# Optimization experiments

Measured on AMD Instinct MI355X. Metric: run time of the kernel, lower is better.

## Reference

```python
import jax, jax.numpy as jnp
import numpy as np
from jax import lax

BATCH, SEQ, IN_DIM, STATE, OUT_DIM = 8, 4096, 256, 256, 256


def setup_inputs() -> dict:
    key = jax.random.key(0)
    kx, ka, kb, kc = jax.random.split(key, 4)
    x = jax.random.normal(kx, (BATCH, SEQ, IN_DIM), dtype=jnp.float32)
    # A initialized as randn normalized by its largest singular value (spectral norm)
    A_init = jax.random.normal(ka, (STATE, STATE), dtype=jnp.float32)
    s_max = jnp.linalg.svd(A_init, compute_uv=False)[0]
    A = A_init / (s_max + 1e-8)
    B = jax.random.normal(kb, (IN_DIM, STATE), dtype=jnp.float32) / IN_DIM
    C = jax.random.normal(kc, (STATE, OUT_DIM), dtype=jnp.float32) / STATE
    h0 = jnp.zeros((STATE,), dtype=jnp.float32)
    return {"x": x, "A": A, "B": B, "C": C, "h0": h0}


def reference(x, A, B, C, h0):
    # h_{t} = h_{t-1} @ A + x_t @ B ;  y_t = h_t @ C
    bsz = x.shape[0]
    xB = jnp.einsum('bsi,in->sbn', x, B)  # precompute input projections, time-major
    h_init = jnp.broadcast_to(h0, (bsz, h0.shape[0]))

    def step(h, xb_t):
        h = h @ A + xb_t
        return h, h

    _, hs = lax.scan(step, h_init, xB)  # hs: [S, B, N]
    y = jnp.einsum('sbn,no->bso', hs, C)  # [B, S, O]
    return y
```

## Files before the change

### kernel.cpp

```cpp
#include <hip/hip_runtime.h>


#define SEQ    4096
#define NBATCH 8
#define ND     256
#define CHUNK  8
#define NCHUNK 512
#define GSZ    16
#define NGRP   32
#define LOSC   2048.0f
#define LOINV  (1.0f/2048.0f)

typedef _Float16 fp16_t;
typedef __attribute__((ext_vector_type(8))) _Float16 f16x8;
typedef __attribute__((ext_vector_type(4))) _Float16 f16x4;
typedef __attribute__((ext_vector_type(4))) float f32x4;

__global__ __launch_bounds__(64) void prep_frags3(
    const float* __restrict__ A, const float* __restrict__ B,
    const float* __restrict__ C,
    fp16_t* __restrict__ fAh, fp16_t* __restrict__ fAl,
    fp16_t* __restrict__ fBh, fp16_t* __restrict__ fBl,
    fp16_t* __restrict__ fCh, fp16_t* __restrict__ fCl) {
  const int which = blockIdx.x >> 7;
  const int blk   = blockIdx.x & 127;
  const float* M = (which == 0) ? A : (which == 1) ? B : C;
  fp16_t* hi = (which == 0) ? fAh : (which == 1) ? fBh : fCh;
  fp16_t* lo = (which == 0) ? fAl : (which == 1) ? fBl : fCl;
  const int lane = threadIdx.x;
  const int tile = blk >> 3, slice = blk & 7;
  const int n  = tile * 16 + (lane & 15);
  const int k0 = slice * 32 + (lane >> 4) * 8;
  f16x8 vh, vl;
  #pragma unroll
  for (int j = 0; j < 8; ++j) {
    const float v = M[(size_t)(k0 + j) * ND + n];
    const fp16_t h = (fp16_t)v;
    vh[j] = h;
    vl[j] = (fp16_t)((v - (float)h) * LOSC);
  }
  const size_t fo = ((size_t)blk * 64 + lane) * 8;
  *(f16x8*)&hi[fo] = vh;
  *(f16x8*)&lo[fo] = vl;
}

__global__ __launch_bounds__(64) void prep_frags2(
    const float* __restrict__ M0, const float* __restrict__ M1,
    fp16_t* __restrict__ h0p, fp16_t* __restrict__ l0p,
    fp16_t* __restrict__ h1p, fp16_t* __restrict__ l1p) {
  const int which = blockIdx.x >> 7;
  const int blk   = blockIdx.x & 127;
  const float* M = (which == 0) ? M0 : M1;
  fp16_t* hi = (which == 0) ? h0p : h1p;
  fp16_t* lo = (which == 0) ? l0p : l1p;
  const int lane = threadIdx.x;
  const int tile = blk >> 3, slice = blk & 7;
  const int n  = tile * 16 + (lane & 15);
  const int k0 = slice * 32 + (lane >> 4) * 8;
  f16x8 vh, vl;
  #pragma unroll
  for (int j = 0; j < 8; ++j) {
    const float v = M[(size_t)(k0 + j) * ND + n];
    const fp16_t h = (fp16_t)v;
    vh[j] = h;
    vl[j] = (fp16_t)((v - (float)h) * LOSC);
  }
  const size_t fo = ((size_t)blk * 64 + lane) * 8;
  *(f16x8*)&hi[fo] = vh;
  *(f16x8*)&lo[fo] = vl;
}

__global__ __launch_bounds__(1024, 4) void mfma_gemm(const float* __restrict__ X,
                                                     const fp16_t* __restrict__ Mhi,
                                                     const fp16_t* __restrict__ Mlo,
                                                     float* __restrict__ Out,
                                                     int mode) {
  const int m0   = blockIdx.x * 64;
  const int tid  = threadIdx.x;
  const int lane = tid & 63;
  const int w    = tid >> 6;
  const int br   = lane & 15;
  const int akg  = lane >> 4;

  __shared__ fp16_t Xh[64 * ND];
  __shared__ fp16_t Xl[64 * ND];
  char* Xhb = (char*)Xh;
  char* Xlb = (char*)Xl;

  {
    const int r0   = tid >> 6;
    const int col0 = (tid & 63) * 4;
    #pragma unroll
    for (int rr = 0; rr < 4; ++rr) {
      const int row = rr * 16 + r0;
      const int m = m0 + row;
      const size_t in_row = (mode == 0)
          ? ((size_t)(m & 7) * SEQ + (m >> 3))
          : (size_t)m;
      const float4 xv = *(const float4*)&X[in_row * ND + col0];
      const float a[4] = {xv.x, xv.y, xv.z, xv.w};
      f16x4 vh, vl;
      #pragma unroll
      for (int j = 0; j < 4; ++j) {
        const fp16_t h = (fp16_t)a[j];
        vh[j] = h;
        vl[j] = (fp16_t)((a[j] - (float)h) * LOSC);
      }
      const int byte = (row * 512 + col0 * 2) ^ ((row & 7) << 4);
      *(f16x4*)(Xhb + byte) = vh;
      *(f16x4*)(Xlb + byte) = vl;
    }
  }

  f16x8 MH[8], ML[8];
  #pragma unroll
  for (int s = 0; s < 8; ++s) {
    const size_t fo = (((size_t)w * 8 + s) * 64 + lane) * 8;
    MH[s] = *(const f16x8*)&Mhi[fo];
    ML[s] = *(const f16x8*)&Mlo[fo];
  }
  __syncthreads();

  f32x4 accm[4], accl[4];
  #pragma unroll
  for (int mt = 0; mt < 4; ++mt) {
    accm[mt] = (f32x4)0.0f;
    accl[mt] = (f32x4)0.0f;
  }

  #pragma unroll
  for (int s = 0; s < 8; ++s) {
    #pragma unroll
    for (int mt = 0; mt < 4; ++mt) {
      const int row = mt * 16 + br;
      const int byte = (row * 512 + s * 64 + akg * 16) ^ ((row & 7) << 4);
      const f16x8 bh = *(const f16x8*)(Xhb + byte);
      const f16x8 bl = *(const f16x8*)(Xlb + byte);
      accm[mt] = __builtin_amdgcn_mfma_f32_16x16x32_f16(MH[s], bh, accm[mt], 0, 0, 0);
      accl[mt] = __builtin_amdgcn_mfma_f32_16x16x32_f16(ML[s], bh, accl[mt], 0, 0, 0);
      accl[mt] = __builtin_amdgcn_mfma_f32_16x16x32_f16(MH[s], bl, accl[mt], 0, 0, 0);
    }
  }

  #pragma unroll
  for (int mt = 0; mt < 4; ++mt) {
    const int m = m0 + mt * 16 + br;
    const size_t out_row = (mode == 1)
        ? ((size_t)(m & 7) * SEQ + (m >> 3))
        : (size_t)m;
    float4 o;
    o.x = accm[mt][0] + accl[mt][0] * LOINV;
    o.y = accm[mt][1] + accl[mt][1] * LOINV;
    o.z = accm[mt][2] + accl[mt][2] * LOINV;
    o.w = accm[mt][3] + accl[mt][3] * LOINV;
    *(float4*)&Out[out_row * ND + w * 16 + akg * 4] = o;
  }
}

__global__ __launch_bounds__(1024, 4) void mfma_rscan(
    const fp16_t* __restrict__ Mh, const fp16_t* __restrict__ Ml,
    const float* __restrict__ Init,
    const float* In,
    float* OutEach,
    float* __restrict__ OutFinal,
    int nupd, int gstride, int nseq, int init_bcast, int entry_mode) {
  const int seq0 = blockIdx.x * 2;
  const int tid  = threadIdx.x;
  const int lane = tid & 63;
  const int w    = tid >> 6;
  const int br   = lane & 15;
  const int akg  = lane >> 4;

  __shared__ fp16_t hH[16 * ND];
  __shared__ fp16_t hL[16 * ND];
  char* hHb = (char*)hH;
  char* hLb = (char*)hL;

  {
    const int row  = tid >> 6;
    const int col0 = (tid & 63) * 4;
    const int sq = seq0 + (row >> 3);
    const int b  = row & 7;
    float4 v = make_float4(0.f, 0.f, 0.f, 0.f);
    if (Init != nullptr && sq < nseq) {
      const size_t off = init_bcast ? (size_t)col0
                                    : ((size_t)sq * NBATCH + b) * ND + col0;
      v = *(const float4*)&Init[off];
      if (entry_mode && OutEach != nullptr)
        *(float4*)&OutEach[((size_t)sq * gstride * NBATCH + b) * ND + col0] = v;
    }
    const float a[4] = {v.x, v.y, v.z, v.w};
    f16x4 vh, vl;
    #pragma unroll
    for (int j = 0; j < 4; ++j) {
      const fp16_t h = (fp16_t)a[j];
      vh[j] = h;
      vl[j] = (fp16_t)((a[j] - (float)h) * LOSC);
    }
    const int byte = (row * 512 + col0 * 2) ^ ((row & 7) << 4);
    *(f16x4*)(hHb + byte) = vh;
    *(f16x4*)(hLb + byte) = vl;
  }

  f16x8 AH[8], AL[8];
  #pragma unroll
  for (int s = 0; s < 8; ++s) {
    const size_t fo = (((size_t)w * 8 + s) * 64 + lane) * 8;
    AH[s] = *(const f16x8*)&Mh[fo];
    AL[s] = *(const f16x8*)&Ml[fo];
  }
  __syncthreads();

  const int sq   = seq0 + (br >> 3);
  const int b    = br & 7;
  const bool live = (sq < nseq);
  const int sqc  = live ? sq : (nseq - 1);
  const int col0 = w * 16 + akg * 4;

  float4 uv = *(const float4*)&In[((size_t)(sqc * gstride) * NBATCH + b) * ND + col0];
  float4 uvn;
  f32x4 res;
  for (int j = 0; j < nupd; ++j) {
    if (j + 1 < nupd)
      uvn = *(const float4*)&In[((size_t)(sqc * gstride + j + 1) * NBATCH + b) * ND + col0];
    f32x4 accm, accl;
    accm[0] = uv.x; accm[1] = uv.y; accm[2] = uv.z; accm[3] = uv.w;
    accl = (f32x4)0.0f;
    #pragma unroll
    for (int s = 0; s < 8; ++s) {
      const int byte = (br * 512 + s * 64 + akg * 16) ^ ((br & 7) << 4);
      const f16x8 bh = *(const f16x8*)(hHb + byte);
      const f16x8 bl = *(const f16x8*)(hLb + byte);
      accm = __builtin_amdgcn_mfma_f32_16x16x32_f16(AH[s], bh, accm, 0, 0, 0);
      accl = __builtin_amdgcn_mfma_f32_16x16x32_f16(AL[s], bh, accl, 0, 0, 0);
      accl = __builtin_amdgcn_mfma_f32_16x16x32_f16(AH[s], bl, accl, 0, 0, 0);
    }
    #pragma unroll
    for (int r = 0; r < 4; ++r) res[r] = accm[r] + accl[r] * LOINV;
    __syncthreads();
    {
      f16x4 vh, vl;
      #pragma unroll
      for (int r = 0; r < 4; ++r) {
        const fp16_t hh = (fp16_t)res[r];
        vh[r] = hh;
        vl[r] = (fp16_t)((res[r] - (float)hh) * LOSC);
      }
      const int wb = (br * 512 + col0 * 2) ^ ((br & 7) << 4);
      *(f16x4*)(hHb + wb) = vh;
      *(f16x4*)(hLb + wb) = vl;
    }
    if (OutEach != nullptr && live) {
      const size_t pos = entry_mode ? (size_t)(sq * gstride + j + 1)
                                    : (size_t)(sq * gstride + j);
      float4 o;
      o.x = res[0]; o.y = res[1]; o.z = res[2]; o.w = res[3];
      *(float4*)&OutEach[(pos * NBATCH + b) * ND + col0] = o;
    }
    uv = uvn;
    __syncthreads();
  }

  if (OutFinal != nullptr && live) {
    float4 o;
    o.x = res[0]; o.y = res[1]; o.z = res[2]; o.w = res[3];
    *(float4*)&OutFinal[((size_t)sq * NBATCH + b) * ND + col0] = o;
  }
}

__global__ __launch_bounds__(256) void gemm256(const float* __restrict__ X,
                                               const float* __restrict__ Y,
                                               float* __restrict__ Out) {
  const int m0 = blockIdx.x * 4;
  const int n  = threadIdx.x;
  __shared__ float Xs[ND][4];
  #pragma unroll
  for (int r = 0; r < 4; ++r) Xs[n][r] = X[(m0 + r) * ND + n];
  __syncthreads();
  float a0 = 0.f, a1 = 0.f, a2 = 0.f, a3 = 0.f;
  #pragma unroll 8
  for (int k = 0; k < ND; ++k) {
    const float yv = Y[k * ND + n];
    const float4 xv = *(const float4*)&Xs[k][0];
    a0 = fmaf(xv.x, yv, a0);
    a1 = fmaf(xv.y, yv, a1);
    a2 = fmaf(xv.z, yv, a2);
    a3 = fmaf(xv.w, yv, a3);
  }
  Out[(m0 + 0) * ND + n] = a0;
  Out[(m0 + 1) * ND + n] = a1;
  Out[(m0 + 2) * ND + n] = a2;
  Out[(m0 + 3) * ND + n] = a3;
}

extern "C" void kernel_launch(void* const* d_in, const int* in_sizes, int n_in,
                              void* d_out, int out_size, void* d_ws, size_t ws_size,
                              hipStream_t stream) {
  const float* x  = (const float*)d_in[0];
  const float* A  = (const float*)d_in[1];
  const float* Bm = (const float*)d_in[2];
  const float* Cm = (const float*)d_in[3];
  const float* h0 = (const float*)d_in[4];
  float* y = (float*)d_out;

  float* U    = (float*)d_ws;
  float* t0   = U + (size_t)SEQ * NBATCH * ND;
  float* t1   = t0 + ND * ND;
  float* A8   = t1 + ND * ND;
  float* A128 = A8 + ND * ND;
  float* E    = A128 + ND * ND;
  float* Sg   = E + (size_t)NCHUNK * NBATCH * ND;
  float* G    = Sg + (size_t)NGRP * NBATCH * ND;
  float* Hc   = G + (size_t)NGRP * NBATCH * ND;
  fp16_t* fA_hi = (fp16_t*)(Hc + (size_t)NCHUNK * NBATCH * ND);
  fp16_t* fA_lo = fA_hi + ND * ND;
  fp16_t* fB_hi = fA_lo + ND * ND;
  fp16_t* fB_lo = fB_hi + ND * ND;
  fp16_t* fC_hi = fB_lo + ND * ND;
  fp16_t* fC_lo = fC_hi + ND * ND;
  fp16_t* fA8_hi   = (fp16_t*)t0;
  fp16_t* fA8_lo   = fA8_hi + ND * ND;
  fp16_t* fA128_hi = (fp16_t*)t1;
  fp16_t* fA128_lo = fA128_hi + ND * ND;

  prep_frags3<<<384, 64, 0, stream>>>(A, Bm, Cm, fA_hi, fA_lo, fB_hi, fB_lo,
                                      fC_hi, fC_lo);

  gemm256<<<64, 256, 0, stream>>>(A,  A,  t0);
  gemm256<<<64, 256, 0, stream>>>(t0, t0, t1);
  gemm256<<<64, 256, 0, stream>>>(t1, t1, A8);
  gemm256<<<64, 256, 0, stream>>>(A8, A8, t0);
  gemm256<<<64, 256, 0, stream>>>(t0, t0, t1);
  gemm256<<<64, 256, 0, stream>>>(t1, t1, t0);
  gemm256<<<64, 256, 0, stream>>>(t0, t0, A128);

  prep_frags2<<<256, 64, 0, stream>>>(A8, A128, fA8_hi, fA8_lo,
                                      fA128_hi, fA128_lo);

  mfma_gemm<<<512, 1024, 0, stream>>>(x, fB_hi, fB_lo, U, 0);

  mfma_rscan<<<NCHUNK / 2, 1024, 0, stream>>>(fA_hi, fA_lo, nullptr, U,
                                              nullptr, E, CHUNK, CHUNK,
                                              NCHUNK, 0, 0);

  mfma_rscan<<<NGRP / 2, 1024, 0, stream>>>(fA8_hi, fA8_lo, nullptr, E,
                                            nullptr, Sg, GSZ, GSZ, NGRP, 0, 0);

  mfma_rscan<<<1, 1024, 0, stream>>>(fA128_hi, fA128_lo, h0, Sg,
                                     G, nullptr, NGRP - 1, NGRP, 1, 1, 1);

  mfma_rscan<<<NGRP / 2, 1024, 0, stream>>>(fA8_hi, fA8_lo, G, E,
                                            Hc, nullptr, GSZ - 1, GSZ, NGRP,
                                            0, 1);

  mfma_rscan<<<NCHUNK / 2, 1024, 0, stream>>>(fA_hi, fA_lo, Hc, U,
                                              U, nullptr, CHUNK, CHUNK,
                                              NCHUNK, 0, 0);

  mfma_gemm<<<512, 1024, 0, stream>>>(U, fC_hi, fC_lo, y, 1);
}
```

Measured before the change: 258.8 us.

## Double-buffer scan state in LDS and re-layout fragments for MFMA reads

The recurrent scan kernel now ping-pongs the fp16 hi/lo state between two LDS buffers, which removes one of the two __syncthreads per step. It also splits the low-part accumulator into two independent chains to shorten the MFMA dependency chain. Both the GEMM and scan kernels change their LDS layout to a per-k-slice, XOR-swizzled fragment-major form so each lane reads a contiguous 16-byte fragment, and the GEMM staging loads 8 floats per thread. The launch-bound occupancy hint is lowered from 4 to 2, which gives the compiler more registers per thread but may reduce residency.

```diff
diff --git a/kernel.cpp b/kernel.cpp
--- a/kernel.cpp
+++ b/kernel.cpp
@@ -70,7 +70,7 @@
   *(f16x8*)&lo[fo] = vl;
 }
 
-__global__ __launch_bounds__(1024, 4) void mfma_gemm(const float* __restrict__ X,
+__global__ __launch_bounds__(1024, 2) void mfma_gemm(const float* __restrict__ X,
                                                      const fp16_t* __restrict__ Mhi,
                                                      const fp16_t* __restrict__ Mlo,
                                                      float* __restrict__ Out,
@@ -82,34 +82,37 @@
   const int br   = lane & 15;
   const int akg  = lane >> 4;
 
-  __shared__ fp16_t Xh[64 * ND];
-  __shared__ fp16_t Xl[64 * ND];
+  __shared__ fp16_t Xh[32 * 512];
+  __shared__ fp16_t Xl[32 * 512];
   char* Xhb = (char*)Xh;
   char* Xlb = (char*)Xl;
 
-  {
-    const int r0   = tid >> 6;
-    const int col0 = (tid & 63) * 4;
-    #pragma unroll
-    for (int rr = 0; rr < 4; ++rr) {
-      const int row = rr * 16 + r0;
-      const int m = m0 + row;
-      const size_t in_row = (mode == 0)
-          ? ((size_t)(m & 7) * SEQ + (m >> 3))
-          : (size_t)m;
-      const float4 xv = *(const float4*)&X[in_row * ND + col0];
-      const float a[4] = {xv.x, xv.y, xv.z, xv.w};
-      f16x4 vh, vl;
-      #pragma unroll
-      for (int j = 0; j < 4; ++j) {
-        const fp16_t h = (fp16_t)a[j];
-        vh[j] = h;
-        vl[j] = (fp16_t)((a[j] - (float)h) * LOSC);
-      }
-      const int byte = (row * 512 + col0 * 2) ^ ((row & 7) << 4);
-      *(f16x4*)(Xhb + byte) = vh;
-      *(f16x4*)(Xlb + byte) = vl;
-    }
+  #pragma unroll
+  for (int pass = 0; pass < 2; ++pass) {
+    const int tau = pass * 1024 + tid;
+    const int row = tau >> 5;
+    const int sub = tau & 31;
+    const int s   = sub >> 2;
+    const int ak  = sub & 3;
+    const int m = m0 + row;
+    const size_t in_row = (mode == 0)
+        ? ((size_t)(m & 7) * SEQ + (m >> 3))
+        : (size_t)m;
+    const float* xp = &X[in_row * ND + s * 32 + ak * 8];
+    const float4 x0 = *(const float4*)(xp);
+    const float4 x1 = *(const float4*)(xp + 4);
+    const float a[8] = {x0.x, x0.y, x0.z, x0.w, x1.x, x1.y, x1.z, x1.w};
+    f16x8 vh, vl;
+    #pragma unroll
+    for (int j = 0; j < 8; ++j) {
+      const fp16_t h = (fp16_t)a[j];
+      vh[j] = h;
+      vl[j] = (fp16_t)((a[j] - (float)h) * LOSC);
+    }
+    const int off = (((row >> 4) * 8 + s) << 10) +
+                    (((ak << 4) | (row & 15)) ^ s) * 16;
+    *(f16x8*)(Xhb + off) = vh;
+    *(f16x8*)(Xlb + off) = vl;
   }
 
   f16x8 MH[8], ML[8];
@@ -128,18 +131,20 @@
     accl[mt] = (f32x4)0.0f;
   }
 
+  const int rdslot = (((akg << 4) | br)) * 16;
   #pragma unroll
   for (int s = 0; s < 8; ++s) {
+    const int rdoff = (s ^ ((rdslot >> 4) & 0)) ;
     #pragma unroll
     for (int mt = 0; mt < 4; ++mt) {
-      const int row = mt * 16 + br;
-      const int byte = (row * 512 + s * 64 + akg * 16) ^ ((row & 7) << 4);
+      const int byte = ((mt * 8 + s) << 10) + ((((akg << 4) | br) ^ s) << 4);
       const f16x8 bh = *(const f16x8*)(Xhb + byte);
       const f16x8 bl = *(const f16x8*)(Xlb + byte);
       accm[mt] = __builtin_amdgcn_mfma_f32_16x16x32_f16(MH[s], bh, accm[mt], 0, 0, 0);
       accl[mt] = __builtin_amdgcn_mfma_f32_16x16x32_f16(ML[s], bh, accl[mt], 0, 0, 0);
       accl[mt] = __builtin_amdgcn_mfma_f32_16x16x32_f16(MH[s], bl, accl[mt], 0, 0, 0);
     }
+    (void)rdoff;
   }
 
   #pragma unroll
@@ -157,7 +162,7 @@
   }
 }
 
-__global__ __launch_bounds__(1024, 4) void mfma_rscan(
+__global__ __launch_bounds__(1024, 2) void mfma_rscan(
     const fp16_t* __restrict__ Mh, const fp16_t* __restrict__ Ml,
     const float* __restrict__ Init,
     const float* In,
@@ -171,23 +176,25 @@
   const int br   = lane & 15;
   const int akg  = lane >> 4;
 
-  __shared__ fp16_t hH[16 * ND];
-  __shared__ fp16_t hL[16 * ND];
-  char* hHb = (char*)hH;
-  char* hLb = (char*)hL;
+  __shared__ fp16_t hH[2][8 * 512];
+  __shared__ fp16_t hL[2][8 * 512];
 
   {
-    const int row  = tid >> 6;
-    const int col0 = (tid & 63) * 4;
+    const int task = tid >> 1;
+    const int half = tid & 1;
+    const int row  = task & 15;
+    const int s    = (task >> 4) & 7;
+    const int ak   = task >> 7;
     const int sq = seq0 + (row >> 3);
     const int b  = row & 7;
+    const int c0 = s * 32 + ak * 8 + half * 4;
     float4 v = make_float4(0.f, 0.f, 0.f, 0.f);
     if (Init != nullptr && sq < nseq) {
-      const size_t off = init_bcast ? (size_t)col0
-                                    : ((size_t)sq * NBATCH + b) * ND + col0;
+      const size_t off = init_bcast ? (size_t)c0
+                                    : ((size_t)sq * NBATCH + b) * ND + c0;
       v = *(const float4*)&Init[off];
       if (entry_mode && OutEach != nullptr)
-        *(float4*)&OutEach[((size_t)sq * gstride * NBATCH + b) * ND + col0] = v;
+        *(float4*)&OutEach[((size_t)sq * gstride * NBATCH + b) * ND + c0] = v;
     }
     const float a[4] = {v.x, v.y, v.z, v.w};
     f16x4 vh, vl;
@@ -197,9 +204,9 @@
       vh[j] = h;
       vl[j] = (fp16_t)((a[j] - (float)h) * LOSC);
     }
-    const int byte = (row * 512 + col0 * 2) ^ ((row & 7) << 4);
-    *(f16x4*)(hHb + byte) = vh;
-    *(f16x4*)(hLb + byte) = vl;
+    const int off = (s << 10) + ((((ak << 4) | row) ^ s) << 4) + half * 8;
+    *(f16x4*)((char*)hH[0] + off) = vh;
+    *(f16x4*)((char*)hL[0] + off) = vl;
   }
 
   f16x8 AH[8], AL[8];
@@ -217,27 +224,37 @@
   const int sqc  = live ? sq : (nseq - 1);
   const int col0 = w * 16 + akg * 4;
 
+  int rdoff[8];
+  #pragma unroll
+  for (int s = 0; s < 8; ++s)
+    rdoff[s] = (s << 10) + ((((akg << 4) | br) ^ s) << 4);
+  const int sw   = col0 >> 5;
+  const int akr  = (col0 >> 3) & 3;
+  const int wroff = (sw << 10) + ((((akr << 4) | br) ^ sw) << 4) + (col0 & 7) * 2;
+
   float4 uv = *(const float4*)&In[((size_t)(sqc * gstride) * NBATCH + b) * ND + col0];
   float4 uvn;
   f32x4 res;
+  int p = 0;
   for (int j = 0; j < nupd; ++j) {
     if (j + 1 < nupd)
       uvn = *(const float4*)&In[((size_t)(sqc * gstride + j + 1) * NBATCH + b) * ND + col0];
-    f32x4 accm, accl;
+    const char* rH = (const char*)hH[p];
+    const char* rL = (const char*)hL[p];
+    f32x4 accm, acclA, acclB;
     accm[0] = uv.x; accm[1] = uv.y; accm[2] = uv.z; accm[3] = uv.w;
-    accl = (f32x4)0.0f;
+    acclA = (f32x4)0.0f;
+    acclB = (f32x4)0.0f;
     #pragma unroll
     for (int s = 0; s < 8; ++s) {
-      const int byte = (br * 512 + s * 64 + akg * 16) ^ ((br & 7) << 4);
-      const f16x8 bh = *(const f16x8*)(hHb + byte);
-      const f16x8 bl = *(const f16x8*)(hLb + byte);
-      accm = __builtin_amdgcn_mfma_f32_16x16x32_f16(AH[s], bh, accm, 0, 0, 0);
-      accl = __builtin_amdgcn_mfma_f32_16x16x32_f16(AL[s], bh, accl, 0, 0, 0);
-      accl = __builtin_amdgcn_mfma_f32_16x16x32_f16(AH[s], bl, accl, 0, 0, 0);
-    }
-    #pragma unroll
-    for (int r = 0; r < 4; ++r) res[r] = accm[r] + accl[r] * LOINV;
-    __syncthreads();
+      const f16x8 bh = *(const f16x8*)(rH + rdoff[s]);
+      const f16x8 bl = *(const f16x8*)(rL + rdoff[s]);
+      accm  = __builtin_amdgcn_mfma_f32_16x16x32_f16(AH[s], bh, accm,  0, 0, 0);
+      acclA = __builtin_amdgcn_mfma_f32_16x16x32_f16(AL[s], bh, acclA, 0, 0, 0);
+      acclB = __builtin_amdgcn_mfma_f32_16x16x32_f16(AH[s], bl, acclB, 0, 0, 0);
+    }
+    #pragma unroll
+    for (int r = 0; r < 4; ++r) res[r] = accm[r] + (acclA[r] + acclB[r]) * LOINV;
     {
       f16x4 vh, vl;
       #pragma unroll
@@ -246,9 +263,8 @@
         vh[r] = hh;
         vl[r] = (fp16_t)((res[r] - (float)hh) * LOSC);
       }
-      const int wb = (br * 512 + col0 * 2) ^ ((br & 7) << 4);
-      *(f16x4*)(hHb + wb) = vh;
-      *(f16x4*)(hLb + wb) = vl;
+      *(f16x4*)((char*)hH[p ^ 1] + wroff) = vh;
+      *(f16x4*)((char*)hL[p ^ 1] + wroff) = vl;
     }
     if (OutEach != nullptr && live) {
       const size_t pos = entry_mode ? (size_t)(sq * gstride + j + 1)
@@ -258,6 +274,7 @@
       *(float4*)&OutEach[(pos * NBATCH + b) * ND + col0] = o;
     }
     uv = uvn;
+    p ^= 1;
     __syncthreads();
   }
 
```

Result: faster. 232.9 us (-10.0%).
